# Optimization experiments

Hardware: AMD Instinct MI355X
Metric: run time of the kernel (lower is better)

The kernel has to match this reference:

```python
import jax, jax.numpy as jnp
import numpy as np

B, L, H = 256, 512, 256      # batch, seq_len, hid_dim
REL_VOCAB = 50000            # relation_input_dim
A = 100000                   # size of global action pool (len(actions))
K = 512                      # action keys per sample (padded ragged dim)
ENT_VOCAB = 40000
PAD = 0                      # entity_pad_idx


def setup_inputs() -> dict:
    key = jax.random.key(0)
    k1, k2, k3, k4, k5, k6 = jax.random.split(key, 6)
    entities = jax.random.randint(k1, (B, L), 0, ENT_VOCAB)
    relations = jax.random.randint(k2, (B, L), 0, REL_VOCAB)
    actions = jax.random.randint(k3, (A,), 0, REL_VOCAB)
    action_keys = jax.random.randint(k4, (B, K), 0, A)
    encoded = jax.random.normal(k5, (B, L, H), dtype=jnp.float32)  # opaque encoder output
    rel_emb = jax.random.normal(k6, (REL_VOCAB, H), dtype=jnp.float32) * 0.02
    return {"entities": entities, "relations": relations, "actions": actions,
            "action_keys": action_keys, "encoded": encoded, "rel_emb": rel_emb}


def reference(entities, relations, actions, action_keys, encoded, rel_emb):
    # mask-based gather of the last non-pad position per sample
    mask = (entities != PAD)                       # [B, L]
    idxs = mask.sum(axis=1) - 1                    # [B]
    enc_last = jnp.take_along_axis(
        encoded, idxs[:, None, None], axis=1).squeeze(1)  # [B, H]
    # only_relations branch: action embedding lookup for the global action pool
    action_emb = rel_emb[actions]                  # [A, H]
    # ragged (padded) per-sample gather + matvec: preds[b,k] = action_emb[keys[b,k]] . enc_last[b]
    gathered = action_emb[action_keys]             # [B, K, H]
    preds = jnp.einsum('bkh,bh->bk', gathered, enc_last)  # [B, K]
    return preds
```

## Files before the change

### kernel.cpp

```cpp
#include <hip/hip_runtime.h>

#define B 256
#define L 512
#define H 256
#define K 512
#define CHUNKS 8
#define KPB (K / CHUNKS)
#define THREADS 256
#define KPW (KPB / 4)
#define KPG (KPW / 4)

__global__ __launch_bounds__(THREADS)
void preds_fused_kernel(const int* __restrict__ entities,
                        const int* __restrict__ actions,
                        const int* __restrict__ action_keys,
                        const float* __restrict__ encoded,
                        const float* __restrict__ rel_emb,
                        float* __restrict__ out)
{
    const int blk   = blockIdx.x;
    const int b     = blk >> 3;
    const int chunk = blk & 7;
    const int t     = threadIdx.x;
    const int lane  = t & 63;
    const int wave  = t >> 6;
    const int gid   = lane >> 4;
    const int gl    = lane & 15;

    __shared__ int s_count;
    if (t == 0) s_count = 0;
    __syncthreads();

    {
        unsigned long long m0 = __ballot(entities[b * L + t] != 0);
        unsigned long long m1 = __ballot(entities[b * L + t + 256] != 0);
        if (lane == 0) atomicAdd(&s_count, __popcll(m0) + __popcll(m1));
    }
    __syncthreads();

    int idx = s_count - 1;
    idx = max(0, min(L - 1, idx));

    const int kw = chunk * KPB + wave * KPW;
    const int* ak = action_keys + b * K;
    int av = 0;
    if (lane < KPW) av = actions[ak[kw + lane]];

    const float* encrow = &encoded[((size_t)(b * L + idx)) * H];
    const float4 e0 = *(const float4*)&encrow[gl * 4];
    const float4 e1 = *(const float4*)&encrow[gl * 4 + 64];
    const float4 e2 = *(const float4*)&encrow[gl * 4 + 128];
    const float4 e3 = *(const float4*)&encrow[gl * 4 + 192];

    #pragma unroll
    for (int i = 0; i < KPG; i += 2) {
        const int o0 = gid * KPG + i;
        const int o1 = o0 + 1;
        const int a0 = __shfl(av, o0, 64);
        const int a1 = __shfl(av, o1, 64);

        const float* r0 = &rel_emb[(size_t)a0 * H];
        const float* r1 = &rel_emb[(size_t)a1 * H];

        float4 r00 = *(const float4*)&r0[gl * 4];
        float4 r01 = *(const float4*)&r0[gl * 4 + 64];
        float4 r02 = *(const float4*)&r0[gl * 4 + 128];
        float4 r03 = *(const float4*)&r0[gl * 4 + 192];
        float4 r10 = *(const float4*)&r1[gl * 4];
        float4 r11 = *(const float4*)&r1[gl * 4 + 64];
        float4 r12 = *(const float4*)&r1[gl * 4 + 128];
        float4 r13 = *(const float4*)&r1[gl * 4 + 192];

        float p0 = r00.x * e0.x + r00.y * e0.y + r00.z * e0.z + r00.w * e0.w;
        p0 += r01.x * e1.x + r01.y * e1.y + r01.z * e1.z + r01.w * e1.w;
        p0 += r02.x * e2.x + r02.y * e2.y + r02.z * e2.z + r02.w * e2.w;
        p0 += r03.x * e3.x + r03.y * e3.y + r03.z * e3.z + r03.w * e3.w;

        float p1 = r10.x * e0.x + r10.y * e0.y + r10.z * e0.z + r10.w * e0.w;
        p1 += r11.x * e1.x + r11.y * e1.y + r11.z * e1.z + r11.w * e1.w;
        p1 += r12.x * e2.x + r12.y * e2.y + r12.z * e2.z + r12.w * e2.w;
        p1 += r13.x * e3.x + r13.y * e3.y + r13.z * e3.z + r13.w * e3.w;

        #pragma unroll
        for (int off = 1; off < 16; off <<= 1) {
            p0 += __shfl_xor(p0, off, 64);
            p1 += __shfl_xor(p1, off, 64);
        }
        if (gl == 0) {
            out[b * K + kw + o0] = p0;
            out[b * K + kw + o1] = p1;
        }
    }
}

extern "C" void kernel_launch(void* const* d_in, const int* in_sizes, int n_in,
                              void* d_out, int out_size, void* d_ws, size_t ws_size,
                              hipStream_t stream)
{
    const int*   entities    = (const int*)d_in[0];
    const int*   actions     = (const int*)d_in[2];
    const int*   action_keys = (const int*)d_in[3];
    const float* encoded     = (const float*)d_in[4];
    const float* rel_emb     = (const float*)d_in[5];
    float*       out         = (float*)d_out;

    hipLaunchKernelGGL(preds_fused_kernel,
                       dim3(B * CHUNKS), dim3(THREADS), 0, stream,
                       entities, actions, action_keys, encoded, rel_emb, out);
}
```

Before: 25.05 us.

## Bin gathers by relation-row range and pin bins to XCDs for L2 locality

Replaces the single fused kernel with two passes. The first pass computes last-token encodings into workspace and buckets every (output index, relation id) pair into 16 bins by relation-id range. The second pass maps bins to XCDs, so each XCD's L2 serves a compact slice of rel_emb when computing the dot products. This trades an extra memset, a second launch, workspace traffic and atomics for better L2 reuse of the embedding table. It also adds a silent overflow risk if a bin holds more than STRIDE entries.

Result: slower. 30.35 us (+21.2%).

```diff
diff --git a/kernel.cpp b/kernel.cpp
--- a/kernel.cpp
+++ b/kernel.cpp
@@ -4,91 +4,151 @@
 #define L 512
 #define H 256
 #define K 512
-#define CHUNKS 8
-#define KPB (K / CHUNKS)
-#define THREADS 256
-#define KPW (KPB / 4)
-#define KPG (KPW / 4)
+#define BINS 16
+#define BINW 3125
+#define STRIDE 12288
 
-__global__ __launch_bounds__(THREADS)
-void preds_fused_kernel(const int* __restrict__ entities,
-                        const int* __restrict__ actions,
-                        const int* __restrict__ action_keys,
-                        const float* __restrict__ encoded,
-                        const float* __restrict__ rel_emb,
-                        float* __restrict__ out)
+#define WS_CNT_OFF 0
+#define WS_ENC_OFF 1024
+#define WS_ENT_OFF (512 * 1024)
+
+__global__ __launch_bounds__(256)
+void passA_bin(const int* __restrict__ entities,
+               const int* __restrict__ actions,
+               const int* __restrict__ action_keys,
+               const float* __restrict__ encoded,
+               float* __restrict__ ws_enc,
+               int* __restrict__ ws_cnt,
+               uint2* __restrict__ ws_ent)
 {
-    const int blk   = blockIdx.x;
-    const int b     = blk >> 3;
-    const int chunk = blk & 7;
-    const int t     = threadIdx.x;
-    const int lane  = t & 63;
-    const int wave  = t >> 6;
-    const int gid   = lane >> 4;
-    const int gl    = lane & 15;
+    const int b    = blockIdx.x;
+    const int t    = threadIdx.x;
+    const int lane = t & 63;
+    const int wave = t >> 6;
 
     __shared__ int s_count;
+    __shared__ int s_wcnt[4][BINS];
+    __shared__ int s_wbase[4][BINS];
+
     if (t == 0) s_count = 0;
+    if (t < 4 * BINS) ((int*)s_wcnt)[t] = 0;
     __syncthreads();
 
-    {
-        unsigned long long m0 = __ballot(entities[b * L + t] != 0);
-        unsigned long long m1 = __ballot(entities[b * L + t + 256] != 0);
-        if (lane == 0) atomicAdd(&s_count, __popcll(m0) + __popcll(m1));
+    unsigned long long m0 = __ballot(entities[b * L + t] != 0);
+    unsigned long long m1 = __ballot(entities[b * L + t + 256] != 0);
+    if (lane == 0) atomicAdd(&s_count, __popcll(m0) + __popcll(m1));
+    __syncthreads();
+    int idx = s_count - 1;
+    idx = max(0, min(L - 1, idx));
+
+    ws_enc[b * H + t] = encoded[((size_t)(b * L + idx)) * H + t];
+
+    const int k0 = t, k1 = t + 256;
+    const int r0 = actions[action_keys[b * K + k0]];
+    const int r1 = actions[action_keys[b * K + k1]];
+    const int bin0 = r0 / BINW;
+    const int bin1 = r1 / BINW;
+
+    const unsigned long long mlt = (lane == 63) ? 0x7FFFFFFFFFFFFFFFull
+                                                : ((1ull << lane) - 1ull);
+    int pos0 = 0, pos1 = 0;
+    #pragma unroll
+    for (int bb = 0; bb < BINS; ++bb) {
+        unsigned long long ma = __ballot(bin0 == bb);
+        unsigned long long mb = __ballot(bin1 == bb);
+        int ca = __popcll(ma);
+        int cb = __popcll(mb);
+        if (lane == 0) s_wcnt[wave][bb] = ca + cb;
+        if (bin0 == bb) pos0 = __popcll(ma & mlt);
+        if (bin1 == bb) pos1 = ca + __popcll(mb & mlt);
     }
     __syncthreads();
 
-    int idx = s_count - 1;
-    idx = max(0, min(L - 1, idx));
+    if (t < BINS) {
+        int tot = 0, basew[4];
+        #pragma unroll
+        for (int w = 0; w < 4; ++w) { basew[w] = tot; tot += s_wcnt[w][t]; }
+        int g = atomicAdd(&ws_cnt[t], tot);
+        #pragma unroll
+        for (int w = 0; w < 4; ++w) s_wbase[w][t] = g + basew[w];
+    }
+    __syncthreads();
 
-    const int kw = chunk * KPB + wave * KPW;
-    const int* ak = action_keys + b * K;
-    int av = 0;
-    if (lane < KPW) av = actions[ak[kw + lane]];
+    const int p0 = s_wbase[wave][bin0] + pos0;
+    const int p1 = s_wbase[wave][bin1] + pos1;
+    if (p0 < STRIDE) ws_ent[bin0 * STRIDE + p0] = make_uint2((unsigned)(b * K + k0), (unsigned)r0);
+    if (p1 < STRIDE) ws_ent[bin1 * STRIDE + p1] = make_uint2((unsigned)(b * K + k1), (unsigned)r1);
+}
 
-    const float* encrow = &encoded[((size_t)(b * L + idx)) * H];
-    const float4 e0 = *(const float4*)&encrow[gl * 4];
-    const float4 e1 = *(const float4*)&encrow[gl * 4 + 64];
-    const float4 e2 = *(const float4*)&encrow[gl * 4 + 128];
-    const float4 e3 = *(const float4*)&encrow[gl * 4 + 192];
+__device__ __forceinline__ float dot4(const float4 a, const float4 b) {
+    return a.x * b.x + a.y * b.y + a.z * b.z + a.w * b.w;
+}
 
-    #pragma unroll
-    for (int i = 0; i < KPG; i += 2) {
-        const int o0 = gid * KPG + i;
-        const int o1 = o0 + 1;
-        const int a0 = __shfl(av, o0, 64);
-        const int a1 = __shfl(av, o1, 64);
+__global__ __launch_bounds__(256)
+void passB_dot(const float* __restrict__ rel_emb,
+               const float* __restrict__ ws_enc,
+               const int* __restrict__ ws_cnt,
+               const uint2* __restrict__ ws_ent,
+               float* __restrict__ out)
+{
+    const int blk   = blockIdx.x;
+    const int xcd   = blk & 7;
+    const int phase = blk >> 11;
+    const int slot  = (blk >> 3) & 255;
+    const int bin   = xcd * 2 + phase;
 
-        const float* r0 = &rel_emb[(size_t)a0 * H];
-        const float* r1 = &rel_emb[(size_t)a1 * H];
+    const int count = min(ws_cnt[bin], STRIDE);
+    const int per_block = (count + 255) >> 8;
+    const int start = slot * per_block;
+    const int end   = min(count, start + per_block);
 
-        float4 r00 = *(const float4*)&r0[gl * 4];
-        float4 r01 = *(const float4*)&r0[gl * 4 + 64];
-        float4 r02 = *(const float4*)&r0[gl * 4 + 128];
-        float4 r03 = *(const float4*)&r0[gl * 4 + 192];
-        float4 r10 = *(const float4*)&r1[gl * 4];
-        float4 r11 = *(const float4*)&r1[gl * 4 + 64];
-        float4 r12 = *(const float4*)&r1[gl * 4 + 128];
-        float4 r13 = *(const float4*)&r1[gl * 4 + 192];
+    const int t    = threadIdx.x;
+    const int lane = t & 63;
+    const int wave = t >> 6;
+    const int gidx = wave * 4 + (lane >> 4);
+    const int gl   = lane & 15;
 
-        float p0 = r00.x * e0.x + r00.y * e0.y + r00.z * e0.z + r00.w * e0.w;
-        p0 += r01.x * e1.x + r01.y * e1.y + r01.z * e1.z + r01.w * e1.w;
-        p0 += r02.x * e2.x + r02.y * e2.y + r02.z * e2.z + r02.w * e2.w;
-        p0 += r03.x * e3.x + r03.y * e3.y + r03.z * e3.z + r03.w * e3.w;
+    const uint2* ebase = ws_ent + bin * STRIDE;
 
-        float p1 = r10.x * e0.x + r10.y * e0.y + r10.z * e0.z + r10.w * e0.w;
-        p1 += r11.x * e1.x + r11.y * e1.y + r11.z * e1.z + r11.w * e1.w;
-        p1 += r12.x * e2.x + r12.y * e2.y + r12.z * e2.z + r12.w * e2.w;
-        p1 += r13.x * e3.x + r13.y * e3.y + r13.z * e3.z + r13.w * e3.w;
+    for (int p = start + gidx * 2; p < end; p += 32) {
+        const bool v1 = (p + 1) < end;
+        const uint2 e0 = ebase[p];
+        const uint2 e1 = v1 ? ebase[p + 1] : e0;
+
+        const float* r0 = &rel_emb[(size_t)e0.y * H];
+        const float* r1 = &rel_emb[(size_t)e1.y * H];
+        const float* q0 = &ws_enc[(e0.x >> 9) * H];
+        const float* q1 = &ws_enc[(e1.x >> 9) * H];
+
+        float4 a0 = *(const float4*)&r0[gl * 4];
+        float4 a1 = *(const float4*)&r0[gl * 4 + 64];
+        float4 a2 = *(const float4*)&r0[gl * 4 + 128];
+        float4 a3 = *(const float4*)&r0[gl * 4 + 192];
+        float4 b0 = *(const float4*)&r1[gl * 4];
+        float4 b1 = *(const float4*)&r1[gl * 4 + 64];
+        float4 b2 = *(const float4*)&r1[gl * 4 + 128];
+        float4 b3 = *(const float4*)&r1[gl * 4 + 192];
+
+        float4 ea0 = *(const float4*)&q0[gl * 4];
+        float4 ea1 = *(const float4*)&q0[gl * 4 + 64];
+        float4 ea2 = *(const float4*)&q0[gl * 4 + 128];
+        float4 ea3 = *(const float4*)&q0[gl * 4 + 192];
+        float4 eb0 = *(const float4*)&q1[gl * 4];
+        float4 eb1 = *(const float4*)&q1[gl * 4 + 64];
+        float4 eb2 = *(const float4*)&q1[gl * 4 + 128];
+        float4 eb3 = *(const float4*)&q1[gl * 4 + 192];
+
+        float s0 = dot4(a0, ea0) + dot4(a1, ea1) + dot4(a2, ea2) + dot4(a3, ea3);
+        float s1 = dot4(b0, eb0) + dot4(b1, eb1) + dot4(b2, eb2) + dot4(b3, eb3);
 
         #pragma unroll
         for (int off = 1; off < 16; off <<= 1) {
-            p0 += __shfl_xor(p0, off, 64);
-            p1 += __shfl_xor(p1, off, 64);
+            s0 += __shfl_xor(s0, off, 64);
+            s1 += __shfl_xor(s1, off, 64);
         }
         if (gl == 0) {
-            out[b * K + kw + o0] = p0;
-            out[b * K + kw + o1] = p1;
+            out[e0.x] = s0;
+            if (v1) out[e1.x] = s1;
         }
     }
 }
@@ -104,7 +164,17 @@
     const float* rel_emb     = (const float*)d_in[5];
     float*       out         = (float*)d_out;
 
-    hipLaunchKernelGGL(preds_fused_kernel,
-                       dim3(B * CHUNKS), dim3(THREADS), 0, stream,
-                       entities, actions, action_keys, encoded, rel_emb, out);
+    char* ws = (char*)d_ws;
+    int*   ws_cnt = (int*)(ws + WS_CNT_OFF);
+    float* ws_enc = (float*)(ws + WS_ENC_OFF);
+    uint2* ws_ent = (uint2*)(ws + WS_ENT_OFF);
+
+    hipMemsetAsync(ws_cnt, 0, BINS * sizeof(int), stream);
+
+    hipLaunchKernelGGL(passA_bin, dim3(B), dim3(256), 0, stream,
+                       entities, actions, action_keys, encoded,
+                       ws_enc, ws_cnt, ws_ent);
+
+    hipLaunchKernelGGL(passB_dot, dim3(BINS * 256), dim3(256), 0, stream,
+                       rel_emb, ws_enc, ws_cnt, ws_ent, out);
 }
```

## Precompute full relation-by-batch score table with bf16 MFMA GEMM, then gather

Applied to the files above, without the earlier changes.

Replaces the per-(b,k) gathered dot products with three kernels. The first casts the last-position encoder row to bf16. The second runs a dense bf16 MFMA GEMM of the whole 50000x256 relation table against the 256 encoder rows and stores a bf16 score table in workspace. The third gathers outputs from that table. This replaces 131k random 1KB row gathers with one streaming read of the table (about 51MB) plus tensor-core compute, at the cost of bf16 precision on inputs and outputs, a roughly 25MB workspace write and two extra launches. The old fused kernel stays as a fallback when the workspace is too small.

New measurement: 62.04 us. 148% more time.

```diff
diff --git a/kernel.cpp b/kernel.cpp
--- a/kernel.cpp
+++ b/kernel.cpp
@@ -4,13 +4,123 @@
 #define L 512
 #define H 256
 #define K 512
+#define RELV 50000
+
+#define WS_ENC_OFF 0
+#define WS_P2_OFF  (256 * 1024)
+#define WS_NEEDED  (WS_P2_OFF + (size_t)RELV * B * 2)
+
+typedef __attribute__((ext_vector_type(8))) short bf16x8;
+typedef __attribute__((ext_vector_type(4))) float f32x4;
+
+__device__ __forceinline__ ushort f2bf(float f) {
+    unsigned u = __float_as_uint(f);
+    u += 0x7fffu + ((u >> 16) & 1u);
+    return (ushort)(u >> 16);
+}
+
+__global__ __launch_bounds__(256)
+void enc_cast(const int* __restrict__ entities,
+              const float* __restrict__ encoded,
+              ushort* __restrict__ encbf)
+{
+    const int b = blockIdx.x, t = threadIdx.x, lane = t & 63;
+    __shared__ int s_count;
+    if (t == 0) s_count = 0;
+    __syncthreads();
+    unsigned long long m0 = __ballot(entities[b * L + t] != 0);
+    unsigned long long m1 = __ballot(entities[b * L + t + 256] != 0);
+    if (lane == 0) atomicAdd(&s_count, __popcll(m0) + __popcll(m1));
+    __syncthreads();
+    int idx = s_count - 1;
+    idx = max(0, min(L - 1, idx));
+    encbf[b * H + t] = f2bf(encoded[((size_t)(b * L + idx)) * H + t]);
+}
+
+__global__ __launch_bounds__(256)
+void gemm_p2(const float* __restrict__ rel_emb,
+             const ushort* __restrict__ encbf,
+             ushort* __restrict__ P2)
+{
+    const int t    = threadIdx.x;
+    const int lane = t & 63;
+    const int w    = t >> 6;
+    const int r0   = blockIdx.x * 64;
+    const int colbase = w * 64;
+    const int lrow = lane & 15;
+    const int lkb  = lane >> 4;
+
+    bf16x8 Bf[8][4];
+    #pragma unroll
+    for (int kb = 0; kb < 8; ++kb)
+        #pragma unroll
+        for (int cf = 0; cf < 4; ++cf) {
+            const ushort* p = encbf + (size_t)(colbase + cf * 16 + lrow) * H
+                            + kb * 32 + lkb * 8;
+            Bf[kb][cf] = *(const bf16x8*)p;
+        }
+
+    #pragma unroll
+    for (int strip = 0; strip < 4; ++strip) {
+        int arow = r0 + strip * 16 + lrow;
+        arow = min(arow, RELV - 1);
+        const float* ap = rel_emb + (size_t)arow * H + lkb * 8;
+
+        f32x4 acc0 = {0.f, 0.f, 0.f, 0.f};
+        f32x4 acc1 = {0.f, 0.f, 0.f, 0.f};
+        f32x4 acc2 = {0.f, 0.f, 0.f, 0.f};
+        f32x4 acc3 = {0.f, 0.f, 0.f, 0.f};
+
+        #pragma unroll
+        for (int kb = 0; kb < 8; ++kb) {
+            float4 a0 = *(const float4*)(ap + kb * 32);
+            float4 a1 = *(const float4*)(ap + kb * 32 + 4);
+            bf16x8 af;
+            af[0] = (short)f2bf(a0.x); af[1] = (short)f2bf(a0.y);
+            af[2] = (short)f2bf(a0.z); af[3] = (short)f2bf(a0.w);
+            af[4] = (short)f2bf(a1.x); af[5] = (short)f2bf(a1.y);
+            af[6] = (short)f2bf(a1.z); af[7] = (short)f2bf(a1.w);
+
+            acc0 = __builtin_amdgcn_mfma_f32_16x16x32_bf16(af, Bf[kb][0], acc0, 0, 0, 0);
+            acc1 = __builtin_amdgcn_mfma_f32_16x16x32_bf16(af, Bf[kb][1], acc1, 0, 0, 0);
+            acc2 = __builtin_amdgcn_mfma_f32_16x16x32_bf16(af, Bf[kb][2], acc2, 0, 0, 0);
+            acc3 = __builtin_amdgcn_mfma_f32_16x16x32_bf16(af, Bf[kb][3], acc3, 0, 0, 0);
+        }
+
+        const int srow = r0 + strip * 16 + lkb * 4;
+        #pragma unroll
+        for (int j = 0; j < 4; ++j) {
+            const int rr = srow + j;
+            if (rr < RELV) {
+                ushort* pr = P2 + (size_t)rr * B + colbase + lrow;
+                pr[0]  = f2bf(acc0[j]);
+                pr[16] = f2bf(acc1[j]);
+                pr[32] = f2bf(acc2[j]);
+                pr[48] = f2bf(acc3[j]);
+            }
+        }
+    }
+}
+
+__global__ __launch_bounds__(256)
+void gather_out(const int* __restrict__ actions,
+                const int* __restrict__ action_keys,
+                const ushort* __restrict__ P2,
+                float* __restrict__ out)
+{
+    const int tid = blockIdx.x * 256 + threadIdx.x;
+    const int b   = tid >> 9;
+    const int r   = actions[action_keys[tid]];
+    const unsigned bits = ((unsigned)P2[(size_t)r * B + b]) << 16;
+    out[tid] = __uint_as_float(bits);
+}
+
 #define CHUNKS 8
 #define KPB (K / CHUNKS)
-#define THREADS 256
 #define KPW (KPB / 4)
 #define KPG (KPW / 4)
 
-__global__ __launch_bounds__(THREADS)
+__global__ __launch_bounds__(256)
 void preds_fused_kernel(const int* __restrict__ entities,
                         const int* __restrict__ actions,
                         const int* __restrict__ action_keys,
@@ -30,14 +140,10 @@
     __shared__ int s_count;
     if (t == 0) s_count = 0;
     __syncthreads();
-
-    {
-        unsigned long long m0 = __ballot(entities[b * L + t] != 0);
-        unsigned long long m1 = __ballot(entities[b * L + t + 256] != 0);
-        if (lane == 0) atomicAdd(&s_count, __popcll(m0) + __popcll(m1));
-    }
-    __syncthreads();
-
+    unsigned long long m0 = __ballot(entities[b * L + t] != 0);
+    unsigned long long m1 = __ballot(entities[b * L + t + 256] != 0);
+    if (lane == 0) atomicAdd(&s_count, __popcll(m0) + __popcll(m1));
+    __syncthreads();
     int idx = s_count - 1;
     idx = max(0, min(L - 1, idx));
 
@@ -58,7 +164,6 @@
         const int o1 = o0 + 1;
         const int a0 = __shfl(av, o0, 64);
         const int a1 = __shfl(av, o1, 64);
-
         const float* r0 = &rel_emb[(size_t)a0 * H];
         const float* r1 = &rel_emb[(size_t)a1 * H];
 
@@ -75,7 +180,6 @@
         p0 += r01.x * e1.x + r01.y * e1.y + r01.z * e1.z + r01.w * e1.w;
         p0 += r02.x * e2.x + r02.y * e2.y + r02.z * e2.z + r02.w * e2.w;
         p0 += r03.x * e3.x + r03.y * e3.y + r03.z * e3.z + r03.w * e3.w;
-
         float p1 = r10.x * e0.x + r10.y * e0.y + r10.z * e0.z + r10.w * e0.w;
         p1 += r11.x * e1.x + r11.y * e1.y + r11.z * e1.z + r11.w * e1.w;
         p1 += r12.x * e2.x + r12.y * e2.y + r12.z * e2.z + r12.w * e2.w;
@@ -104,7 +208,18 @@
     const float* rel_emb     = (const float*)d_in[5];
     float*       out         = (float*)d_out;
 
-    hipLaunchKernelGGL(preds_fused_kernel,
-                       dim3(B * CHUNKS), dim3(THREADS), 0, stream,
-                       entities, actions, action_keys, encoded, rel_emb, out);
-}
+    if (ws_size >= WS_NEEDED) {
+        ushort* encbf = (ushort*)((char*)d_ws + WS_ENC_OFF);
+        ushort* P2    = (ushort*)((char*)d_ws + WS_P2_OFF);
+
+        hipLaunchKernelGGL(enc_cast, dim3(B), dim3(256), 0, stream,
+                           entities, encoded, encbf);
+        hipLaunchKernelGGL(gemm_p2, dim3((RELV + 63) / 64), dim3(256), 0, stream,
+                           rel_emb, encbf, P2);
+        hipLaunchKernelGGL(gather_out, dim3(B * K / 256), dim3(256), 0, stream,
+                           actions, action_keys, P2, out);
+    } else {
+        hipLaunchKernelGGL(preds_fused_kernel, dim3(B * CHUNKS), dim3(256), 0, stream,
+                           entities, actions, action_keys, encoded, rel_emb, out);
+    }
+}
```
